# Performance work log

Hardware: AMD Instinct MI355X
Metric: run time of the kernel (lower is better)

The kernel has to match this reference:

```python
import jax, jax.numpy as jnp
import numpy as np
from jax import lax

DIMS = 64
MARGIN = 0.85
NENT = 400000
NREL = 512
B = 1024
NNEG = 255


def setup_inputs() -> dict:
    key = jax.random.key(0)
    ks = jax.random.split(key, 9)
    d = DIMS
    positive_sample = jax.random.randint(ks[0], (B, 3), 0, NREL, dtype=jnp.int32)
    negative_sample = jax.random.randint(ks[1], (B, NNEG), 0, NENT, dtype=jnp.int32)
    emb_entity = jax.random.normal(ks[2], (NENT, d), jnp.float32) * (1.0 / np.float32(np.sqrt(d)))
    bias_head = 0.1 * jax.random.normal(ks[3], (NENT,), jnp.float32)
    bias_tail = 0.1 * jax.random.normal(ks[4], (NENT,), jnp.float32)
    rot_w_head = jax.random.normal(ks[5], (NREL, (d - 1) * (d - 1)), jnp.float32)
    boost_w_head = jax.random.normal(ks[6], (NREL, d - 1), jnp.float32)
    rot_w_tail = jax.random.normal(ks[7], (NREL, (d - 1) * (d - 1)), jnp.float32)
    boost_w_tail = jax.random.normal(ks[8], (NREL, d - 1), jnp.float32)
    return {
        'positive_sample': positive_sample,
        'negative_sample': negative_sample,
        'emb_entity': emb_entity,
        'bias_head': bias_head,
        'bias_tail': bias_tail,
        'rot_w_head': rot_w_head,
        'boost_w_head': boost_w_head,
        'rot_w_tail': rot_w_tail,
        'boost_w_tail': boost_w_tail,
    }


def _orthogonal(w_raw, d):
    # gelu(weight) rows -> product of (d-1) Householder reflections per relation
    vv = jax.nn.gelu(w_raw, approximate=False).reshape(-1, d - 1, d - 1)  # [R, d-1, d-1]
    R = vv.shape[0]
    eye = jnp.eye(d - 1, dtype=vv.dtype)
    def step(Iw, v):  # Iw [R,d-1,d-1], v [R,d-1]
        n = jnp.sum(v * v, axis=-1)[:, None, None]           # [R,1,1]
        Q = eye - 2.0 * (v[:, :, None] * v[:, None, :]) / n  # [R,d-1,d-1]
        return jnp.einsum('rij,rjk->rik', Iw, Q), None
    Iw0 = jnp.tile(eye[None], (R, 1, 1))
    Iw, _ = lax.scan(step, Iw0, jnp.swapaxes(vv, 0, 1))
    return Iw


def _rotation(x, r_idx, rot_w, d):
    W = _orthogonal(rot_w, d)[r_idx]                         # [B,d-1,d-1]
    x0 = x[..., :1]
    xn = jnp.einsum('bnd,bdc->bnc', x[..., 1:], W)
    return jnp.concatenate([x0, xn], axis=-1)


def _boost(x, r_idx, boost_w, d):
    r_o = jnp.tanh(boost_w[r_idx]) / np.float32(d)           # [B,d-1]
    v2 = jnp.sum(r_o * r_o, axis=-1)[:, None, None]          # [B,1,1]
    zeta = 1.0 / (jnp.sqrt(1.0 - v2) + 1e-8)                 # [B,1,1]
    t = x[..., :1]                                           # [B,n,1]
    r = x[..., 1:]                                           # [B,n,d-1]
    rro = r_o[:, None, :]                                    # [B,1,d-1]
    dot = jnp.sum(r * rro, axis=-1, keepdims=True)           # [B,n,1]
    x0 = zeta * t - zeta * dot
    xr = -zeta * t * rro + r + (zeta - 1.0) / (v2 + 1e-9) * rro * dot
    return jnp.concatenate([x0, xr], axis=-1)


def reference(positive_sample, negative_sample, emb_entity, bias_head, bias_tail,
              rot_w_head, boost_w_head, rot_w_tail, boost_w_tail):
    d = DIMS
    u = positive_sample[:, 0]
    r_idx = positive_sample[:, 1]
    v = jnp.concatenate([positive_sample[:, 2:3], negative_sample], axis=1)  # [B,N]
    h = emb_entity[u][:, None, :]                            # [B,1,d]
    t = emb_entity[v]                                        # [B,N,d]
    th = _boost(_rotation(h, r_idx, rot_w_head, d), r_idx, boost_w_head, d)  # [B,1,d]
    tt = _boost(_rotation(t, r_idx, rot_w_tail, d), r_idx, boost_w_tail, d)  # [B,N,d]
    dt = tt - th
    mkv = -dt[..., 0] ** 2 + jnp.sum(dt[..., 1:] ** 2, axis=-1)  # Lorentz cinner2, [B,N]
    # eval mode: noise term is zero
    return MARGIN - mkv + jnp.tanh(bias_head[u])[:, None] + jnp.tanh(bias_tail[v])
```

## Files before the change

kernel.cpp:

```cpp
#include <hip/hip_runtime.h>
#include <math.h>

#define DM1 63
#define VSTR 68

typedef float f4 __attribute__((ext_vector_type(4)));

#define OFF_WRO 0u
#define SZ_WRO  (512u*64u)
#define OFF_WTH (OFF_WRO + SZ_WRO)
#define SZ_WTH  (1024u*64u)
#define OFF_TC  (OFF_WTH + SZ_WTH)
#define SZ_TC   (1024u*4u)
#define OFF_ZK  (OFF_TC + SZ_TC)

__device__ __forceinline__ float qreduce(float d) {
    int t = __builtin_amdgcn_mov_dpp(__float_as_int(d), 0xB1, 0xF, 0xF, true);
    d += __int_as_float(t);
    t = __builtin_amdgcn_mov_dpp(__float_as_int(d), 0x4E, 0xF, 0xF, true);
    d += __int_as_float(t);
    return d;
}

__device__ __forceinline__ float qbcast0(float x) {
    return __int_as_float(__builtin_amdgcn_mov_dpp(__float_as_int(x), 0x00, 0xF, 0xF, true));
}

__device__ __forceinline__ float wred(float x) {
    float s = x;
#define ST(ctrl, rmask) s += __int_as_float(__builtin_amdgcn_update_dpp( \
        0, __float_as_int(s), ctrl, rmask, 0xF, true))
    ST(0x111, 0xF);
    ST(0x112, 0xF);
    ST(0x114, 0xF);
    ST(0x118, 0xF);
    ST(0x142, 0xA);
    ST(0x143, 0xC);
#undef ST
    return __int_as_float(__builtin_amdgcn_readlane(__float_as_int(s), 63));
}

__global__ __launch_bounds__(512) void k_prep(const float* __restrict__ rwh,
                                              const float* __restrict__ rwt,
                                              const float* __restrict__ bwh,
                                              const float* __restrict__ bwt,
                                              const int* __restrict__ pos,
                                              const float* __restrict__ emb,
                                              const float* __restrict__ bh,
                                              float* __restrict__ wrog,
                                              float* __restrict__ wthg,
                                              float* __restrict__ thcg,
                                              float* __restrict__ zkg) {
    int r = blockIdx.x;
    __shared__ __align__(16) float vvh[DM1 * VSTR];
    __shared__ __align__(16) float vvt[DM1 * VSTR];
    __shared__ float sch[64], sct[64];
    __shared__ float rovh_s[64], rovt_s[64];
    __shared__ float hcons[2];
    __shared__ int blist[64];
    __shared__ int bcnt;
    int tid = threadIdx.x;
    if (tid == 0) bcnt = 0;

    const float* rwhr = rwh + (size_t)r * 3969;
    const float* rwtr = rwt + (size_t)r * 3969;
    for (int idx = tid; idx < 3969; idx += 512) {
        int s = idx / 63, j = idx - s * 63;
        float xh = rwhr[idx], xt = rwtr[idx];
        vvh[s * VSTR + j] = 0.5f * xh * (1.f + erff(xh * 0.70710678118654752f));
        vvt[s * VSTR + j] = 0.5f * xt * (1.f + erff(xt * 0.70710678118654752f));
    }
    if (tid < DM1) { vvh[tid * VSTR + 63] = 0.f; vvt[tid * VSTR + 63] = 0.f; }

    if (tid < 64) {
        int c = tid;
        float rov = (c < 63) ? tanhf(bwh[r * 63 + c]) * 0.015625f : 0.f;
        rovh_s[c] = rov;
        float p = rov * rov;
        #pragma unroll
        for (int off = 32; off; off >>= 1) p += __shfl_xor(p, off);
        if (c == 0) {
            float v2 = p;
            float zeta = 1.f / (sqrtf(1.f - v2) + 1e-8f);
            hcons[0] = zeta;
            hcons[1] = (zeta - 1.f) / (v2 + 1e-9f);
        }
    } else if (tid < 128) {
        int c = tid - 64;
        float rov = (c < 63) ? tanhf(bwt[r * 63 + c]) * 0.015625f : 0.f;
        rovt_s[c] = rov;
        float p = rov * rov;
        #pragma unroll
        for (int off = 32; off; off >>= 1) p += __shfl_xor(p, off);
        if (c == 0) {
            float v2 = p;
            float zeta = 1.f / (sqrtf(1.f - v2) + 1e-8f);
            zkg[r * 4]     = zeta;
            zkg[r * 4 + 1] = (zeta - 1.f) / (v2 + 1e-9f);
            zkg[r * 4 + 2] = v2;
        }
    }
    __syncthreads();

    if (tid < 252) {
        int s = tid >> 2, p = tid & 3;
        const float* vr = &vvh[s * VSTR + p * 16];
        float sum = 0.f;
        #pragma unroll
        for (int j = 0; j < 16; j++) { float v = vr[j]; sum = fmaf(v, v, sum); }
        sum = qreduce(sum);
        if (p == 0) sch[s] = sqrtf(2.f / sum);
        const float* vr2 = &vvt[s * VSTR + p * 16];
        float sum2 = 0.f;
        #pragma unroll
        for (int j = 0; j < 16; j++) { float v = vr2[j]; sum2 = fmaf(v, v, sum2); }
        sum2 = qreduce(sum2);
        if (p == 0) sct[s] = sqrtf(2.f / sum2);
    }
    for (int i = tid; i < 1024; i += 512)
        if (pos[3 * i + 1] == r) { int s = atomicAdd(&bcnt, 1); if (s < 64) blist[s] = i; }
    __syncthreads();

    for (int idx = tid; idx < DM1 * 64; idx += 512) {
        int s = idx >> 6, j = idx & 63;
        vvh[s * VSTR + j] *= sch[s];
        vvt[s * VSTR + j] *= sct[s];
    }
    __syncthreads();

    int lane = tid & 63, wv = tid >> 6;
    int cnt = bcnt < 64 ? bcnt : 64;
    float zeta_h = hcons[0], kz_h = hcons[1];

    if (wv == 0) {
        float y = rovt_s[lane];
        float vs = vvt[62 * VSTR + lane];
        #pragma unroll 7
        for (int s = 62; s >= 0; s--) {
            float vn = (s > 0) ? vvt[(s - 1) * VSTR + lane] : 0.f;
            float dot = wred(y * vs);
            y = fmaf(-dot, vs, y);
            vs = vn;
        }
        if (lane < 63) wrog[r * 64 + 1 + lane] = y;
        else           wrog[r * 64] = 0.f;
    } else {
        for (int e = wv - 1; e < cnt; e += 7) {
            int b = blist[e];
            int u = pos[3 * b];
            const float* hrow = emb + (size_t)u * 64;
            float x0 = hrow[0];
            float y = (lane < 63) ? hrow[1 + lane] : 0.f;
            float vs = vvh[0 * VSTR + lane];
            #pragma unroll 7
            for (int s = 0; s < 63; s++) {
                float vn = (s < 62) ? vvh[(s + 1) * VSTR + lane] : 0.f;
                float dot = wred(y * vs);
                y = fmaf(-dot, vs, y);
                vs = vn;
            }
            float rh = rovh_s[lane];
            float dot = wred(y * rh);
            float th1 = (lane < 63) ? fmaf(-zeta_h * x0, rh, y) + kz_h * rh * dot : 0.f;
            float th0 = zeta_h * x0 - zeta_h * dot;
            float nn = wred(th1 * th1);
            float qq = wred(th1 * rovt_s[lane]);
            if (lane == 0) {
                thcg[b * 4]     = th0;
                thcg[b * 4 + 1] = nn;
                thcg[b * 4 + 2] = qq;
                thcg[b * 4 + 3] = tanhf(bh[u]);
            }
            float z = th1;
            float ws2 = vvt[62 * VSTR + lane];
            #pragma unroll 7
            for (int s = 62; s >= 0; s--) {
                float wn = (s > 0) ? vvt[(s - 1) * VSTR + lane] : 0.f;
                float d2 = wred(z * ws2);
                z = fmaf(-d2, ws2, z);
                ws2 = wn;
            }
            if (lane < 63) wthg[b * 64 + 1 + lane] = z;
            else           wthg[b * 64] = 0.f;
        }
    }
}

__global__ __launch_bounds__(256) void k3_score(
    const int* __restrict__ pos, const int* __restrict__ neg,
    const float* __restrict__ emb, const float* __restrict__ bt,
    const float* __restrict__ wrog, const float* __restrict__ wthg,
    const float* __restrict__ thcg, const float* __restrict__ zkg,
    float* __restrict__ out) {
    __shared__ __align__(16) float wro_s[64];
    __shared__ __align__(16) float wth_s[64];
    __shared__ float cst[7];

    int b = blockIdx.x, j = threadIdx.x;
    int r = pos[b * 3 + 1];
    int qslot = j >> 2, p = j & 3;

    if (j < 16)            ((f4*)wro_s)[j]      = ((const f4*)(wrog + r * 64))[j];
    else if (j < 32)       ((f4*)wth_s)[j - 16] = ((const f4*)(wthg + b * 64))[j - 16];
    else if (j == 32)      { cst[0] = zkg[r * 4]; cst[1] = zkg[r * 4 + 1]; cst[2] = zkg[r * 4 + 2]; }
    else if (j == 33)      { const float* tc = thcg + b * 4;
                             cst[3] = tc[0]; cst[4] = tc[1]; cst[5] = tc[2]; cst[6] = tc[3]; }
    __syncthreads();

    float zeta = cst[0], kk = cst[1], v2 = cst[2];
    float th0 = cst[3], nrm = cst[4], qd = cst[5], bhu = cst[6];
    const f4* wr4 = (const f4*)wro_s + p * 4;
    const f4* wt4 = (const f4*)wth_s + p * 4;

    #pragma unroll
    for (int cc = 0; cc < 4; cc++) {
        int cand = cc * 64 + qslot;
        int v = (cand == 0) ? pos[b * 3 + 2] : neg[b * 255 + cand - 1];
        const f4* tp = (const f4*)(emb + (size_t)v * 64) + p * 4;
        f4 t0 = tp[0], t1 = tp[1], t2 = tp[2], t3 = tp[3];
        float btv = bt[v];

        float x0 = qbcast0(t0[0]);
        f4 a1 = t0 * wr4[0] + t1 * wr4[1] + t2 * wr4[2] + t3 * wr4[3];
        f4 a2 = t0 * wt4[0] + t1 * wt4[1] + t2 * wt4[2] + t3 * wt4[3];
        f4 a3 = t0 * t0 + t1 * t1 + t2 * t2 + t3 * t3;
        float s1 = qreduce((a1[0] + a1[1]) + (a1[2] + a1[3]));
        float s2 = qreduce((a2[0] + a2[1]) + (a2[2] + a2[3]));
        float s3 = qreduce((a3[0] + a3[1]) + (a3[2] + a3[3])) - x0 * x0;

        float A  = fmaf(kk, s1, -zeta * x0);
        float d0 = fmaf(zeta, x0 - s1, -th0);
        float m1 = s3 + nrm - 2.f * s2 + A * (2.f * (s1 - qd) + A * v2);
        float mkv = m1 - d0 * d0;
        if (p == 0) out[b * 256 + cand] = 0.85f - mkv + bhu + tanhf(btv);
    }
}

extern "C" void kernel_launch(void* const* d_in, const int* in_sizes, int n_in,
                              void* d_out, int out_size, void* d_ws, size_t ws_size,
                              hipStream_t stream) {
    const int*   pos = (const int*)d_in[0];
    const int*   neg = (const int*)d_in[1];
    const float* emb = (const float*)d_in[2];
    const float* bh  = (const float*)d_in[3];
    const float* bt  = (const float*)d_in[4];
    const float* rwh = (const float*)d_in[5];
    const float* bwh = (const float*)d_in[6];
    const float* rwt = (const float*)d_in[7];
    const float* bwt = (const float*)d_in[8];
    float* ws   = (float*)d_ws;
    float* wrog = ws + OFF_WRO;
    float* wthg = ws + OFF_WTH;
    float* thcg = ws + OFF_TC;
    float* zkg  = ws + OFF_ZK;
    float* out  = (float*)d_out;

    k_prep  <<<dim3(512),  dim3(512), 0, stream>>>(rwh, rwt, bwh, bwt, pos, emb,
                                                   bh, wrog, wthg, thcg, zkg);
    k3_score<<<dim3(1024), dim3(256), 0, stream>>>(pos, neg, emb, bt, wrog, wthg,
                                                   thcg, zkg, out);
}
```

Baseline: 38.38 us.

## Pack four Householder chains per wave with 16-lane reductions; split scoring blocks

In the prep kernel, each Householder sequence now runs on a 16-lane group that holds four elements per lane, so one wave handles four entities at once. The old 64-lane DPP reduction with a readlane becomes a 16-lane DPP reduction, and the wrog row computation is folded into the same rounds as the per-entity chains. The scoring kernel splits each batch row across two blocks of 128 candidates and adds an occupancy hint to launch_bounds. This aims to shorten the serial reflection chains and raise parallelism, at the cost of more redundant per-block setup loads.

```diff
diff --git a/kernel.cpp b/kernel.cpp
--- a/kernel.cpp
+++ b/kernel.cpp
@@ -26,18 +26,17 @@
     return __int_as_float(__builtin_amdgcn_mov_dpp(__float_as_int(x), 0x00, 0xF, 0xF, true));
 }
 
-__device__ __forceinline__ float wred(float x) {
-    float s = x;
-#define ST(ctrl, rmask) s += __int_as_float(__builtin_amdgcn_update_dpp( \
-        0, __float_as_int(s), ctrl, rmask, 0xF, true))
-    ST(0x111, 0xF);
-    ST(0x112, 0xF);
-    ST(0x114, 0xF);
-    ST(0x118, 0xF);
-    ST(0x142, 0xA);
-    ST(0x143, 0xC);
-#undef ST
-    return __int_as_float(__builtin_amdgcn_readlane(__float_as_int(s), 63));
+__device__ __forceinline__ float red16(float d) {
+    d += __int_as_float(__builtin_amdgcn_mov_dpp(__float_as_int(d), 0xB1,  0xF, 0xF, true));
+    d += __int_as_float(__builtin_amdgcn_mov_dpp(__float_as_int(d), 0x4E,  0xF, 0xF, true));
+    d += __int_as_float(__builtin_amdgcn_mov_dpp(__float_as_int(d), 0x124, 0xF, 0xF, true));
+    d += __int_as_float(__builtin_amdgcn_mov_dpp(__float_as_int(d), 0x128, 0xF, 0xF, true));
+    return d;
+}
+
+__device__ __forceinline__ float dot4(f4 a, f4 b) {
+    f4 p = a * b;
+    return (p[0] + p[1]) + (p[2] + p[3]);
 }
 
 __global__ __launch_bounds__(512) void k_prep(const float* __restrict__ rwh,
@@ -55,7 +54,7 @@
     __shared__ __align__(16) float vvh[DM1 * VSTR];
     __shared__ __align__(16) float vvt[DM1 * VSTR];
     __shared__ float sch[64], sct[64];
-    __shared__ float rovh_s[64], rovt_s[64];
+    __shared__ __align__(16) float rovh_s[64], rovt_s[64];
     __shared__ float hcons[2];
     __shared__ int blist[64];
     __shared__ int bcnt;
@@ -129,64 +128,78 @@
     __syncthreads();
 
     int lane = tid & 63, wv = tid >> 6;
+    int g = lane >> 4, c = lane & 15;
     int cnt = bcnt < 64 ? bcnt : 64;
     float zeta_h = hcons[0], kz_h = hcons[1];
 
-    if (wv == 0) {
-        float y = rovt_s[lane];
-        float vs = vvt[62 * VSTR + lane];
+    int rounds = (cnt + 30) / 31; if (rounds < 1) rounds = 1;
+    for (int rd = 0; rd < rounds; rd++) {
+        int gslot = wv * 4 + g;
+        bool iswro = (rd == 0) && (gslot == 0);
+        int eslot = rd * 31 + gslot - 1;
+        bool isent = (gslot > 0) && (eslot < cnt);
+        int bb = isent ? blist[eslot] : 0;
+        int u  = pos[3 * bb];
+        const float* hrow = emb + (size_t)u * 64;
+
+        f4 a = ((const f4*)hrow)[c];
+        float an0 = __shfl(a[0], lane + 1);
+        f4 y;
+        y[0] = a[1]; y[1] = a[2]; y[2] = a[3];
+        y[3] = (c == 15) ? 0.f : an0;
+        if (!isent) y = (f4)0.f;
+        float x0 = hrow[0];
+
+        #pragma unroll 7
+        for (int s = 0; s < 63; s++) {
+            f4 vs = *(const f4*)(&vvh[s * VSTR + 4 * c]);
+            float dot = red16(dot4(y, vs));
+            y -= dot * vs;
+        }
+
+        f4 rh4 = ((const f4*)rovh_s)[c];
+        f4 rt4 = ((const f4*)rovt_s)[c];
+        float dot = red16(dot4(y, rh4));
+        f4 th1 = y + (-zeta_h * x0) * rh4 + (kz_h * dot) * rh4;
+        float th0 = zeta_h * x0 - zeta_h * dot;
+        float nn = red16(dot4(th1, th1));
+        float qq = red16(dot4(th1, rt4));
+        if (isent && c == 0) {
+            thcg[bb * 4]     = th0;
+            thcg[bb * 4 + 1] = nn;
+            thcg[bb * 4 + 2] = qq;
+            thcg[bb * 4 + 3] = tanhf(bh[u]);
+        }
+
+        f4 z = isent ? th1 : (iswro ? rt4 : (f4)0.f);
         #pragma unroll 7
         for (int s = 62; s >= 0; s--) {
-            float vn = (s > 0) ? vvt[(s - 1) * VSTR + lane] : 0.f;
-            float dot = wred(y * vs);
-            y = fmaf(-dot, vs, y);
-            vs = vn;
-        }
-        if (lane < 63) wrog[r * 64 + 1 + lane] = y;
-        else           wrog[r * 64] = 0.f;
-    } else {
-        for (int e = wv - 1; e < cnt; e += 7) {
-            int b = blist[e];
-            int u = pos[3 * b];
-            const float* hrow = emb + (size_t)u * 64;
-            float x0 = hrow[0];
-            float y = (lane < 63) ? hrow[1 + lane] : 0.f;
-            float vs = vvh[0 * VSTR + lane];
-            #pragma unroll 7
-            for (int s = 0; s < 63; s++) {
-                float vn = (s < 62) ? vvh[(s + 1) * VSTR + lane] : 0.f;
-                float dot = wred(y * vs);
-                y = fmaf(-dot, vs, y);
-                vs = vn;
+            f4 vs = *(const f4*)(&vvt[s * VSTR + 4 * c]);
+            float d2 = red16(dot4(z, vs));
+            z -= d2 * vs;
+        }
+
+        if (isent) {
+            float* wo = wthg + bb * 64;
+            if (c == 0) wo[0] = 0.f;
+            #pragma unroll
+            for (int k = 0; k < 4; k++) {
+                int idx = 4 * c + k;
+                if (idx < 63) wo[1 + idx] = z[k];
             }
-            float rh = rovh_s[lane];
-            float dot = wred(y * rh);
-            float th1 = (lane < 63) ? fmaf(-zeta_h * x0, rh, y) + kz_h * rh * dot : 0.f;
-            float th0 = zeta_h * x0 - zeta_h * dot;
-            float nn = wred(th1 * th1);
-            float qq = wred(th1 * rovt_s[lane]);
-            if (lane == 0) {
-                thcg[b * 4]     = th0;
-                thcg[b * 4 + 1] = nn;
-                thcg[b * 4 + 2] = qq;
-                thcg[b * 4 + 3] = tanhf(bh[u]);
+        } else if (iswro) {
+            float* wo = wrog + r * 64;
+            if (c == 0) wo[0] = 0.f;
+            #pragma unroll
+            for (int k = 0; k < 4; k++) {
+                int idx = 4 * c + k;
+                if (idx < 63) wo[1 + idx] = z[k];
             }
-            float z = th1;
-            float ws2 = vvt[62 * VSTR + lane];
-            #pragma unroll 7
-            for (int s = 62; s >= 0; s--) {
-                float wn = (s > 0) ? vvt[(s - 1) * VSTR + lane] : 0.f;
-                float d2 = wred(z * ws2);
-                z = fmaf(-d2, ws2, z);
-                ws2 = wn;
-            }
-            if (lane < 63) wthg[b * 64 + 1 + lane] = z;
-            else           wthg[b * 64] = 0.f;
-        }
-    }
-}
-
-__global__ __launch_bounds__(256) void k3_score(
+        }
+    }
+}
+
+__global__ __launch_bounds__(256, 6) void k3_score(
     const int* __restrict__ pos, const int* __restrict__ neg,
     const float* __restrict__ emb, const float* __restrict__ bt,
     const float* __restrict__ wrog, const float* __restrict__ wthg,
@@ -196,7 +209,9 @@
     __shared__ __align__(16) float wth_s[64];
     __shared__ float cst[7];
 
-    int b = blockIdx.x, j = threadIdx.x;
+    int blk = blockIdx.x;
+    int b = blk >> 1, half = blk & 1;
+    int j = threadIdx.x;
     int r = pos[b * 3 + 1];
     int qslot = j >> 2, p = j & 3;
 
@@ -213,8 +228,8 @@
     const f4* wt4 = (const f4*)wth_s + p * 4;
 
     #pragma unroll
-    for (int cc = 0; cc < 4; cc++) {
-        int cand = cc * 64 + qslot;
+    for (int cc = 0; cc < 2; cc++) {
+        int cand = half * 128 + cc * 64 + qslot;
         int v = (cand == 0) ? pos[b * 3 + 2] : neg[b * 255 + cand - 1];
         const f4* tp = (const f4*)(emb + (size_t)v * 64) + p * 4;
         f4 t0 = tp[0], t1 = tp[1], t2 = tp[2], t3 = tp[3];
@@ -257,6 +272,6 @@
 
     k_prep  <<<dim3(512),  dim3(512), 0, stream>>>(rwh, rwt, bwh, bwt, pos, emb,
                                                    bh, wrog, wthg, thcg, zkg);
-    k3_score<<<dim3(1024), dim3(256), 0, stream>>>(pos, neg, emb, bt, wrog, wthg,
+    k3_score<<<dim3(2048), dim3(256), 0, stream>>>(pos, neg, emb, bt, wrog, wthg,
                                                    thcg, zkg, out);
 }
```

New measurement: 43.24 us. 1.13x slower.
